# Kernel tuning notes

Hardware: AMD Instinct MI355X
Metric: run time of the kernel (lower is better)

Reference implementation:

```python
import jax, jax.numpy as jnp
import numpy as np

IN_CAP_N = 1152   # 128*3*3
IN_CAP_SZ = 5
OUT_CAP_N = 55
OUT_CAP_SZ = 1
BATCH = 8192
ROUTING_ITERS = 2


def setup_inputs() -> dict:
    key = jax.random.key(0)
    k_u, k_w = jax.random.split(key)
    u = jax.random.normal(k_u, (BATCH, IN_CAP_SZ, 128, 3, 3), dtype=jnp.float32)
    W = jax.random.normal(k_w, (1, IN_CAP_N, OUT_CAP_SZ), dtype=jnp.float32)
    b = jnp.zeros((OUT_CAP_N, OUT_CAP_SZ), dtype=jnp.float32)
    return {"u": u, "W": W, "b": b}


def _squash(s):
    # s: (B, 55, 1)
    norm_sq = jnp.sum(s * s, axis=2, keepdims=True)
    norm = jnp.sqrt(norm_sq)
    return norm / (1.0 + norm_sq) * s


def reference(u, W, b):
    B = u.shape[0]
    u_ = u.reshape(B, IN_CAP_SZ, IN_CAP_N)              # (B, 5, 1152)
    u_hat = jnp.matmul(u_, jnp.broadcast_to(W, (B, IN_CAP_N, OUT_CAP_SZ)))  # (B, 5, 1)
    # routing logits, expanded from (55,1) param to (B, 55, 5)
    b_ij = jnp.broadcast_to(b, (B, OUT_CAP_N, IN_CAP_SZ))
    v = None
    for _ in range(ROUTING_ITERS):
        c = jax.nn.softmax(b_ij, axis=1)                 # softmax over out-capsules
        s = jnp.matmul(c, u_hat)                         # (B, 55, 5)@(B, 5, 1) -> (B, 55, 1)
        v = _squash(s)
        b_ij = b_ij + jnp.matmul(v, jnp.swapaxes(u_hat, 1, 2))  # (B, 55, 5)
    return v
```

## Files before the change

kernel.cpp:

```cpp
#include <hip/hip_runtime.h>
#include <math.h>

#define IN_CAP_N   1152
#define ROW_F4     288
#define IN_CAP_SZ  5
#define OUT_CAP_N  55
#define NBATCH     8192
#define WAVES_PER_BLOCK 4

__global__ __launch_bounds__(256) void digitcaps_fused(
    const float* __restrict__ u,
    const float* __restrict__ W,
    const float* __restrict__ bparam,
    float* __restrict__ out)
{
    const int lane = threadIdx.x & 63;
    const int wave = threadIdx.x >> 6;
    const int b    = blockIdx.x * WAVES_PER_BLOCK + wave;

    const float4* W4 = (const float4*)W;
    float4 wreg[5];
    #pragma unroll
    for (int p = 0; p < 4; ++p) wreg[p] = W4[p * 64 + lane];
    wreg[4] = (lane < 32) ? W4[256 + lane] : make_float4(0.f, 0.f, 0.f, 0.f);

    const float4* u4 = (const float4*)(u + (size_t)b * (IN_CAP_SZ * IN_CAP_N));
    float h[IN_CAP_SZ];
    #pragma unroll
    for (int i = 0; i < IN_CAP_SZ; ++i) {
        const float4* row = u4 + i * ROW_F4;
        float acc = 0.f;
        #pragma unroll
        for (int p = 0; p < 4; ++p) {
            float4 uv = row[p * 64 + lane];
            acc += uv.x * wreg[p].x + uv.y * wreg[p].y
                 + uv.z * wreg[p].z + uv.w * wreg[p].w;
        }
        if (lane < 32) {
            float4 uv = row[256 + lane];
            acc += uv.x * wreg[4].x + uv.y * wreg[4].y
                 + uv.z * wreg[4].z + uv.w * wreg[4].w;
        }
        #pragma unroll
        for (int off = 32; off > 0; off >>= 1)
            acc += __shfl_xor(acc, off, 64);
        h[i] = acc;
    }

    const bool active = (lane < OUT_CAP_N);
    float binit = active ? bparam[lane] : 0.f;
    float bij[IN_CAP_SZ];
    #pragma unroll
    for (int i = 0; i < IN_CAP_SZ; ++i) bij[i] = binit;

    float v = 0.f;
    #pragma unroll
    for (int it = 0; it < 2; ++it) {
        float c[IN_CAP_SZ];
        #pragma unroll
        for (int i = 0; i < IN_CAP_SZ; ++i) {
            float x = active ? bij[i] : -INFINITY;
            float m = x;
            #pragma unroll
            for (int off = 32; off > 0; off >>= 1)
                m = fmaxf(m, __shfl_xor(m, off, 64));
            float e = active ? __expf(bij[i] - m) : 0.f;
            float sum = e;
            #pragma unroll
            for (int off = 32; off > 0; off >>= 1)
                sum += __shfl_xor(sum, off, 64);
            c[i] = e / sum;
        }
        float s = 0.f;
        #pragma unroll
        for (int i = 0; i < IN_CAP_SZ; ++i) s += c[i] * h[i];
        v = fabsf(s) * s / (1.f + s * s);
        #pragma unroll
        for (int i = 0; i < IN_CAP_SZ; ++i) bij[i] += v * h[i];
    }
    if (active) out[(size_t)b * OUT_CAP_N + lane] = v;
}

extern "C" void kernel_launch(void* const* d_in, const int* in_sizes, int n_in,
                              void* d_out, int out_size, void* d_ws, size_t ws_size,
                              hipStream_t stream) {
    const float* u  = (const float*)d_in[0];
    const float* W  = (const float*)d_in[1];
    const float* bp = (const float*)d_in[2];
    float* out = (float*)d_out;
    digitcaps_fused<<<NBATCH / WAVES_PER_BLOCK, WAVES_PER_BLOCK * 64, 0, stream>>>(u, W, bp, out);
}
```

Baseline: 262.7 us.

## Preload all u rows with nontemporal float2 loads and batch wave reductions

Switches u and W access from float4 with a half-wave tail to nine float2 loads per lane, with no divergent tail. All five rows are issued up front as nontemporal loads so more memory requests are in flight at once. The five per-row shuffle reductions and the softmax reductions are interleaved so their latencies overlap. The first routing iteration is simplified using the shared initial logits. The cost is more live registers (45 float2 for u) and narrower loads, which may hurt occupancy or load efficiency.

```diff
diff --git a/kernel.cpp b/kernel.cpp
--- a/kernel.cpp
+++ b/kernel.cpp
@@ -2,11 +2,13 @@
 #include <math.h>
 
 #define IN_CAP_N   1152
-#define ROW_F4     288
+#define ROW_F2     576
 #define IN_CAP_SZ  5
 #define OUT_CAP_N  55
 #define NBATCH     8192
 #define WAVES_PER_BLOCK 4
+
+typedef float f32x2 __attribute__((ext_vector_type(2)));
 
 __global__ __launch_bounds__(256) void digitcaps_fused(
     const float* __restrict__ u,
@@ -18,67 +20,83 @@
     const int wave = threadIdx.x >> 6;
     const int b    = blockIdx.x * WAVES_PER_BLOCK + wave;
 
-    const float4* W4 = (const float4*)W;
-    float4 wreg[5];
+    const f32x2* W2 = (const f32x2*)W;
+    f32x2 wreg[9];
     #pragma unroll
-    for (int p = 0; p < 4; ++p) wreg[p] = W4[p * 64 + lane];
-    wreg[4] = (lane < 32) ? W4[256 + lane] : make_float4(0.f, 0.f, 0.f, 0.f);
+    for (int p = 0; p < 9; ++p) wreg[p] = W2[p * 64 + lane];
 
-    const float4* u4 = (const float4*)(u + (size_t)b * (IN_CAP_SZ * IN_CAP_N));
+    const f32x2* u2 = (const f32x2*)(u + (size_t)b * (IN_CAP_SZ * IN_CAP_N));
+    f32x2 uv[IN_CAP_SZ][9];
+    #pragma unroll
+    for (int i = 0; i < IN_CAP_SZ; ++i) {
+        const f32x2* row = u2 + i * ROW_F2;
+        #pragma unroll
+        for (int p = 0; p < 9; ++p)
+            uv[i][p] = __builtin_nontemporal_load(&row[p * 64 + lane]);
+    }
+
     float h[IN_CAP_SZ];
     #pragma unroll
     for (int i = 0; i < IN_CAP_SZ; ++i) {
-        const float4* row = u4 + i * ROW_F4;
-        float acc = 0.f;
+        float a0 = 0.f, a1 = 0.f;
         #pragma unroll
-        for (int p = 0; p < 4; ++p) {
-            float4 uv = row[p * 64 + lane];
-            acc += uv.x * wreg[p].x + uv.y * wreg[p].y
-                 + uv.z * wreg[p].z + uv.w * wreg[p].w;
+        for (int p = 0; p < 9; ++p) {
+            a0 += uv[i][p].x * wreg[p].x;
+            a1 += uv[i][p].y * wreg[p].y;
         }
-        if (lane < 32) {
-            float4 uv = row[256 + lane];
-            acc += uv.x * wreg[4].x + uv.y * wreg[4].y
-                 + uv.z * wreg[4].z + uv.w * wreg[4].w;
-        }
+        h[i] = a0 + a1;
+    }
+    #pragma unroll
+    for (int off = 32; off > 0; off >>= 1) {
         #pragma unroll
-        for (int off = 32; off > 0; off >>= 1)
-            acc += __shfl_xor(acc, off, 64);
-        h[i] = acc;
+        for (int i = 0; i < IN_CAP_SZ; ++i)
+            h[i] += __shfl_xor(h[i], off, 64);
     }
 
     const bool active = (lane < OUT_CAP_N);
-    float binit = active ? bparam[lane] : 0.f;
-    float bij[IN_CAP_SZ];
+    const float b0 = active ? bparam[lane] : -INFINITY;
+
+    float m = b0;
     #pragma unroll
-    for (int i = 0; i < IN_CAP_SZ; ++i) bij[i] = binit;
+    for (int off = 32; off > 0; off >>= 1)
+        m = fmaxf(m, __shfl_xor(m, off, 64));
+    float e = active ? __expf(b0 - m) : 0.f;
+    float sum = e;
+    #pragma unroll
+    for (int off = 32; off > 0; off >>= 1)
+        sum += __shfl_xor(sum, off, 64);
+    const float c1 = e / sum;
+    const float hs = h[0] + h[1] + h[2] + h[3] + h[4];
+    float s = c1 * hs;
+    float v = fabsf(s) * s / (1.f + s * s);
 
-    float v = 0.f;
+    float x[IN_CAP_SZ], mm[IN_CAP_SZ], ee[IN_CAP_SZ], ss[IN_CAP_SZ];
     #pragma unroll
-    for (int it = 0; it < 2; ++it) {
-        float c[IN_CAP_SZ];
+    for (int i = 0; i < IN_CAP_SZ; ++i) { x[i] = b0 + v * h[i]; mm[i] = x[i]; }
+    #pragma unroll
+    for (int off = 32; off > 0; off >>= 1) {
         #pragma unroll
-        for (int i = 0; i < IN_CAP_SZ; ++i) {
-            float x = active ? bij[i] : -INFINITY;
-            float m = x;
-            #pragma unroll
-            for (int off = 32; off > 0; off >>= 1)
-                m = fmaxf(m, __shfl_xor(m, off, 64));
-            float e = active ? __expf(bij[i] - m) : 0.f;
-            float sum = e;
-            #pragma unroll
-            for (int off = 32; off > 0; off >>= 1)
-                sum += __shfl_xor(sum, off, 64);
-            c[i] = e / sum;
-        }
-        float s = 0.f;
+        for (int i = 0; i < IN_CAP_SZ; ++i)
+            mm[i] = fmaxf(mm[i], __shfl_xor(mm[i], off, 64));
+    }
+    #pragma unroll
+    for (int i = 0; i < IN_CAP_SZ; ++i)
+        ee[i] = active ? __expf(x[i] - mm[i]) : 0.f;
+    #pragma unroll
+    for (int i = 0; i < IN_CAP_SZ; ++i) ss[i] = ee[i];
+    #pragma unroll
+    for (int off = 32; off > 0; off >>= 1) {
         #pragma unroll
-        for (int i = 0; i < IN_CAP_SZ; ++i) s += c[i] * h[i];
-        v = fabsf(s) * s / (1.f + s * s);
-        #pragma unroll
-        for (int i = 0; i < IN_CAP_SZ; ++i) bij[i] += v * h[i];
+        for (int i = 0; i < IN_CAP_SZ; ++i)
+            ss[i] += __shfl_xor(ss[i], off, 64);
     }
-    if (active) out[(size_t)b * OUT_CAP_N + lane] = v;
+    s = 0.f;
+    #pragma unroll
+    for (int i = 0; i < IN_CAP_SZ; ++i) s += (ee[i] / ss[i]) * h[i];
+    v = fabsf(s) * s / (1.f + s * s);
+
+    if (active)
+        __builtin_nontemporal_store(v, &out[(size_t)b * OUT_CAP_N + lane]);
 }
 
 extern "C" void kernel_launch(void* const* d_in, const int* in_sizes, int n_in,
```

After: 245.1 us. 6.7% less time.
